# Optimization experiments

Measured on AMD Instinct MI355X. Metric: run time of the kernel, lower is better.

Reference implementation:

```python
import jax, jax.numpy as jnp
import numpy as np
from jax import lax

B, C, H, W = 32, 3, 32, 32
F = 160      # nr_filters
NBLK = 5     # nr_resnet
NMIX = 10    # mixture components
P = 100      # nr_params for 3-channel input


def concat_elu(x):
    return jax.nn.elu(jnp.concatenate([x, -x], axis=1))


def _conv(x, w, b, pad):
    y = lax.conv_general_dilated(x, w, (1, 1), pad, dimension_numbers=('NCHW', 'OIHW', 'NCHW'))
    return y + b[None, :, None, None]


def ds_conv(x, w, b):
    # down-shifted conv: causal in vertical direction
    kh, kw = w.shape[2], w.shape[3]
    return _conv(x, w, b, ((kh - 1, 0), ((kw - 1) // 2, (kw - 1) // 2)))


def dr_conv(x, w, b):
    # down-right-shifted conv: causal in vertical and horizontal direction
    kh, kw = w.shape[2], w.shape[3]
    return _conv(x, w, b, ((kh - 1, 0), (kw - 1, 0)))


def down_shift(x):
    return jnp.pad(x, ((0, 0), (0, 0), (1, 0), (0, 0)))[:, :, :-1, :]


def right_shift(x):
    return jnp.pad(x, ((0, 0), (0, 0), (0, 0), (1, 0)))[:, :, :, :-1]


def nin(x, w, b):
    return jnp.einsum('bchw,oc->bohw', x, w) + b[None, :, None, None]


def gated_resnet(x, a, c1w, c1b, ninw, ninb, c2w, c2b, conv_fn):
    c1 = conv_fn(concat_elu(x), c1w, c1b)
    if a is not None:
        c1 = c1 + nin(concat_elu(a), ninw, ninb)
    c2 = conv_fn(concat_elu(c1), c2w, c2b)  # 2F channels
    g1, g2 = jnp.split(c2, 2, axis=1)
    return x + g1 * jax.nn.sigmoid(g2)


def dmll(x, l):
    # discretized mixture logistic loss; x: [B,C,H,W] in [-1,1], l: [B,P,H,W]
    x = jnp.transpose(x, (0, 2, 3, 1))   # BHWC
    l = jnp.transpose(l, (0, 2, 3, 1))   # BHWP
    logit_probs = l[..., :NMIX]
    rest = l[..., NMIX:].reshape(l.shape[:3] + (C, 3 * NMIX))
    means = rest[..., :NMIX]
    log_scales = jnp.maximum(rest[..., NMIX:2 * NMIX], -7.0)
    coeffs = jnp.tanh(rest[..., 2 * NMIX:])
    xe = x[..., None]                    # BHWC1
    m1 = means[..., 0, :]
    m2 = means[..., 1, :] + coeffs[..., 0, :] * xe[..., 0, :]
    m3 = means[..., 2, :] + coeffs[..., 1, :] * xe[..., 0, :] + coeffs[..., 2, :] * xe[..., 1, :]
    means = jnp.stack([m1, m2, m3], axis=3)  # BHWCM
    centered = xe - means
    inv_stdv = jnp.exp(-log_scales)
    plus_in = inv_stdv * (centered + 1.0 / 255.0)
    min_in = inv_stdv * (centered - 1.0 / 255.0)
    cdf_delta = jax.nn.sigmoid(plus_in) - jax.nn.sigmoid(min_in)
    log_cdf_plus = plus_in - jax.nn.softplus(plus_in)
    log_one_minus_cdf_min = -jax.nn.softplus(min_in)
    mid_in = inv_stdv * centered
    log_pdf_mid = mid_in - log_scales - 2.0 * jax.nn.softplus(mid_in)
    log_probs = jnp.where(xe < -0.999, log_cdf_plus,
                jnp.where(xe > 0.999, log_one_minus_cdf_min,
                jnp.where(cdf_delta > 1e-5, jnp.log(jnp.maximum(cdf_delta, 1e-12)),
                          log_pdf_mid - np.float32(np.log(127.5)))))
    log_probs = log_probs.sum(axis=3) + jax.nn.log_softmax(logit_probs, axis=-1)
    return -jnp.sum(jax.nn.logsumexp(log_probs, axis=-1))


def _forward(samples, w_u_init, b_u_init, w_ul_d, b_ul_d, w_ul_dr, b_ul_dr,
             u_c1_w, u_c1_b, u_c2_w, u_c2_b,
             ul_c1_w, ul_c1_b, ul_nin_w, ul_nin_b, ul_c2_w, ul_c2_b,
             nin_out_w, nin_out_b):
    x = samples * 2.0 - 1.0
    # PixelCNN++ pads a constant ones channel onto the input
    xp = jnp.concatenate([x, jnp.ones_like(x[:, :1])], axis=1)
    u = down_shift(ds_conv(xp, w_u_init, b_u_init))
    ul = down_shift(ds_conv(xp, w_ul_d, b_ul_d)) + right_shift(dr_conv(xp, w_ul_dr, b_ul_dr))
    for i in range(NBLK):
        u = gated_resnet(u, None, u_c1_w[i], u_c1_b[i], None, None, u_c2_w[i], u_c2_b[i], ds_conv)
        ul = gated_resnet(ul, u, ul_c1_w[i], ul_c1_b[i], ul_nin_w[i], ul_nin_b[i], ul_c2_w[i], ul_c2_b[i], dr_conv)
    params = nin(jax.nn.elu(ul), nin_out_w, nin_out_b)  # [B,P,H,W]
    return -dmll(x, params)  # log_prob (scalar, summed over batch/pixels)


def setup_inputs() -> dict:
    key = jax.random.key(0)
    ks = jax.random.split(key, 12)
    s = 0.05
    return {
        'samples': jax.random.uniform(ks[0], (B, C, H, W), jnp.float32),
        'w_u_init': jax.random.normal(ks[1], (F, C + 1, 2, 3), jnp.float32) * s,
        'b_u_init': jnp.zeros((F,), jnp.float32),
        'w_ul_d': jax.random.normal(ks[2], (F, C + 1, 1, 3), jnp.float32) * s,
        'b_ul_d': jnp.zeros((F,), jnp.float32),
        'w_ul_dr': jax.random.normal(ks[3], (F, C + 1, 2, 1), jnp.float32) * s,
        'b_ul_dr': jnp.zeros((F,), jnp.float32),
        'u_c1_w': jax.random.normal(ks[4], (NBLK, F, 2 * F, 2, 3), jnp.float32) * s,
        'u_c1_b': jnp.zeros((NBLK, F), jnp.float32),
        'u_c2_w': jax.random.normal(ks[5], (NBLK, 2 * F, 2 * F, 2, 3), jnp.float32) * s,
        'u_c2_b': jnp.zeros((NBLK, 2 * F), jnp.float32),
        'ul_c1_w': jax.random.normal(ks[6], (NBLK, F, 2 * F, 2, 2), jnp.float32) * s,
        'ul_c1_b': jnp.zeros((NBLK, F), jnp.float32),
        'ul_nin_w': jax.random.normal(ks[7], (NBLK, F, 2 * F), jnp.float32) * s,
        'ul_nin_b': jnp.zeros((NBLK, F), jnp.float32),
        'ul_c2_w': jax.random.normal(ks[8], (NBLK, 2 * F, 2 * F, 2, 2), jnp.float32) * s,
        'ul_c2_b': jnp.zeros((NBLK, 2 * F), jnp.float32),
        'nin_out_w': jax.random.normal(ks[9], (P, F), jnp.float32) * s,
        'nin_out_b': jnp.zeros((P,), jnp.float32),
    }


def reference(samples, w_u_init, b_u_init, w_ul_d, b_ul_d, w_ul_dr, b_ul_dr,
              u_c1_w, u_c1_b, u_c2_w, u_c2_b,
              ul_c1_w, ul_c1_b, ul_nin_w, ul_nin_b, ul_c2_w, ul_c2_b,
              nin_out_w, nin_out_b):
    return _forward(samples, w_u_init, b_u_init, w_ul_d, b_ul_d, w_ul_dr, b_ul_dr,
                    u_c1_w, u_c1_b, u_c2_w, u_c2_b,
                    ul_c1_w, ul_c1_b, ul_nin_w, ul_nin_b, ul_c2_w, ul_c2_b,
                    nin_out_w, nin_out_b)
```

## Files before the change

### kernel.cpp

```cpp
#include <hip/hip_runtime.h>
#include <math.h>

#define BZ 32
#define FCH 160
#define NMIX 10
#define PCH 100

typedef __attribute__((ext_vector_type(8))) short bf16x8;
typedef __attribute__((ext_vector_type(8))) unsigned short u16x8;
typedef __attribute__((ext_vector_type(4))) unsigned short u16x4;
typedef __attribute__((ext_vector_type(4))) float f32x4;

__device__ __forceinline__ unsigned short f2bf(float f) {
    union { float f; unsigned u; } x; x.f = f;
    return (unsigned short)((x.u + 0x7FFFu + ((x.u >> 16) & 1u)) >> 16);
}
__device__ __forceinline__ void elupair(float v, float& e0, float& e1) {
    if (v > 0.f) { e0 = v; e1 = expm1f(-v); }
    else         { e0 = expm1f(v); e1 = -v; }
}
__device__ __forceinline__ int fsw(int p) { return (p + (p >> 2)) & 3; }
__device__ __forceinline__ int swz(int p, int seg) {
    return p * 32 + ((seg ^ fsw(p)) << 3);
}
__device__ __forceinline__ void load_lds16(const unsigned short* g, unsigned short* l) {
    __builtin_amdgcn_global_load_lds(
        (const __attribute__((address_space(1))) unsigned int*)g,
        (__attribute__((address_space(3))) unsigned int*)l, 16, 0, 0);
}

__global__ __launch_bounds__(256) void repack_k(
    const float* __restrict__ w, unsigned short* __restrict__ wb,
    int Cout, int Cin, int NT, int ILV)
{
    __shared__ float ws[1920];
    const int o = blockIdx.x;
    const int nb = blockIdx.y;
    const int CoutPad = gridDim.x;
    const int n = Cin * NT;
    unsigned short* dst = wb + (size_t)(nb * CoutPad + o) * n;
    if (o >= Cout) {
        for (int e = threadIdx.x; e < n; e += 256) dst[e] = 0;
        return;
    }
    const float* src = w + (size_t)(nb * Cout + o) * n;
    for (int e = threadIdx.x; e < n; e += 256) ws[e] = src[e];
    __syncthreads();
    const int half = Cin >> 1;
    for (int e = threadIdx.x; e < n; e += 256) {
        int tap = e / Cin;
        int k = e - tap * Cin;
        int csrc = ILV ? ((k & 1) ? (half + (k >> 1)) : (k >> 1)) : k;
        dst[e] = f2bf(ws[csrc * NT + tap]);
    }
}

__global__ __launch_bounds__(256) void init_both_k(
    const float* __restrict__ smp,
    const float* __restrict__ wu_g, const float* __restrict__ bu_g,
    const float* __restrict__ wd_g, const float* __restrict__ bd_g,
    const float* __restrict__ wr_g, const float* __restrict__ br_g,
    float* __restrict__ u, float* __restrict__ ul,
    unsigned short* __restrict__ ceu, unsigned short* __restrict__ ceul,
    float* __restrict__ zg)
{
    __shared__ float wU[160 * 24];
    __shared__ float wD[160 * 12];
    __shared__ float wR[160 * 8];
    __shared__ float bU[160], bD[160], bR[160];
    __shared__ float X[3][4][34];

    const int tid = threadIdx.x;
    const int i = blockIdx.x;
    const int b = blockIdx.y;

    if (i == 0 && b == 0 && tid < 128) {
        f32x4 z = {0.f, 0.f, 0.f, 0.f};
        ((f32x4*)zg)[tid] = z;
    }

    for (int e = tid; e < 160 * 24; e += 256) wU[e] = wu_g[e];
    for (int e = tid; e < 160 * 12; e += 256) wD[e] = wd_g[e];
    for (int e = tid; e < 160 * 8;  e += 256) wR[e] = wr_g[e];
    if (tid < 160) { bU[tid] = bu_g[tid]; bD[tid] = bd_g[tid]; bR[tid] = br_g[tid]; }
    for (int e = tid; e < 3 * 4 * 34; e += 256) {
        int col = e % 34;
        int c = (e / 34) & 3;
        int rs = e / (34 * 4);
        int r = i - 2 + rs;
        int jj = col - 1;
        float v = 0.f;
        if ((unsigned)r < 32u && (unsigned)jj < 32u)
            v = (c < 3) ? (smp[(((size_t)b * 3 + c) << 10) + (r << 5) + jj] * 2.f - 1.f)
                        : 1.f;
        X[rs][c][col] = v;
    }
    __syncthreads();
    if (tid >= 160) return;
    const int o = tid;

    float wu_r[24], wd_r[12], wr_r[8];
#pragma unroll
    for (int q = 0; q < 24; ++q) wu_r[q] = wU[o * 24 + q];
#pragma unroll
    for (int q = 0; q < 12; ++q) wd_r[q] = wD[o * 12 + q];
#pragma unroll
    for (int q = 0; q < 8; ++q)  wr_r[q] = wR[o * 8 + q];
    const float bu_v = (i > 0) ? bU[o] : 0.f;
    const float bd_v = (i >= 1) ? bD[o] : 0.f;
    const float br_v = bR[o];

    for (int j = 0; j < 32; ++j) {
        float su = 0.f, sd = 0.f, sr = 0.f;
#pragma unroll
        for (int c = 0; c < 4; ++c) {
            float x00 = X[0][c][j], x01 = X[0][c][j + 1], x02 = X[0][c][j + 2];
            float x10 = X[1][c][j], x11 = X[1][c][j + 1], x12 = X[1][c][j + 2];
            float x20 = X[2][c][j];
            su += wu_r[c * 6 + 0] * x00 + wu_r[c * 6 + 1] * x01 + wu_r[c * 6 + 2] * x02
                + wu_r[c * 6 + 3] * x10 + wu_r[c * 6 + 4] * x11 + wu_r[c * 6 + 5] * x12;
            sd += wd_r[c * 3 + 0] * x10 + wd_r[c * 3 + 1] * x11 + wd_r[c * 3 + 2] * x12;
            sr += wr_r[c * 2 + 0] * x10 + wr_r[c * 2 + 1] * x20;
        }
        float uv = (i > 0) ? (su + bu_v) : 0.f;
        float ulv = sd + bd_v + sr + ((j >= 1) ? br_v : 0.f);

        size_t base = (size_t)((b << 10) | (i << 5) | j);
        u[base * 160 + o] = uv;
        ul[base * 160 + o] = ulv;
        float e0, e1;
        elupair(uv, e0, e1);
        unsigned pu = (unsigned)f2bf(e0) | ((unsigned)f2bf(e1) << 16);
        *(unsigned*)(ceu + base * 320 + 2 * o) = pu;
        elupair(ulv, e0, e1);
        unsigned pl = (unsigned)f2bf(e0) | ((unsigned)f2bf(e1) << 16);
        *(unsigned*)(ceul + base * 320 + 2 * o) = pl;
    }
}

template<int KH, int KW, int PT, int PL, bool DUAL, bool GATE, int MBLK>
__global__ __launch_bounds__(256) void conv_mfma_k(
    const unsigned short* __restrict__ cein,
    const unsigned short* __restrict__ wb,
    const unsigned short* __restrict__ cein2,
    const unsigned short* __restrict__ wb2,
    const float* __restrict__ bias, const float* __restrict__ bias2,
    float* __restrict__ resid,
    unsigned short* __restrict__ ceout,
    const unsigned short* __restrict__ zguard)
{
    constexpr int NT = KH * KW;
    constexpr int RW = 8 + KH - 1;
    constexpr int CW = 32 + KW - 1;
    constexpr int MTILES = MBLK / 16;
    constexpr int MSH = (MBLK == 32) ? 5 : 6;
    constexpr int NSA = NT * MBLK / 64;
    constexpr int NSB = (RW * CW * 4 + 255) / 256;

    __shared__ __align__(16) unsigned short bs[NSB * 64 * 32];
    __shared__ __align__(16) unsigned short wsm[NT * MBLK * 32];

    const int tid = threadIdx.x;
    const int wv = tid >> 6;
    const int lane = tid & 63;
    const int l16 = lane & 15;
    const int quad = lane >> 4;

    const int bid = blockIdx.x;
    const int q8 = bid >> 3;
    const int yt = (bid & 7) * 16 + q8 / 5;
    const int m0 = (q8 % 5) * 32;
    const int bimg = yt >> 2;
    const int rowbase = (yt & 3) * 8;

    const int sd = lane & 3;
    const int lr = lane >> 2;

    const unsigned short* srcA[NSA];
#pragma unroll
    for (int it = 0; it < NSA; ++it) {
        int row = it * 64 + wv * 16 + lr;
        int tap = row >> MSH;
        int mm = row & (MBLK - 1);
        int o = GATE ? (mm < 32 ? m0 + mm : 128 + m0 + mm) : (m0 + mm);
        int ss = sd ^ fsw(row);
        srcA[it] = wb + ((size_t)o * NT + tap) * 320 + ss * 8;
    }
    const unsigned short* srcB[NSB];
#pragma unroll
    for (int it = 0; it < NSB; ++it) {
        int p = it * 64 + wv * 16 + lr;
        int r = p / CW;
        int c = p - r * CW;
        int grow = rowbase + r - PT;
        int gcol = c - PL;
        int ss = sd ^ fsw(p);
        bool ok = (p < RW * CW) && ((unsigned)grow < 32u) && ((unsigned)gcol < 32u);
        srcB[it] = ok ? cein + (size_t)(((bimg << 10) | (grow << 5) | gcol)) * 320 + ss * 8
                      : zguard;
    }

    f32x4 acc[MTILES][4];
#pragma unroll
    for (int mt = 0; mt < MTILES; ++mt)
#pragma unroll
        for (int ng = 0; ng < 4; ++ng)
#pragma unroll
            for (int r = 0; r < 4; ++r) acc[mt][ng][r] = 0.f;

    for (int k0 = 0; k0 < 320; k0 += 32) {
        __syncthreads();
#pragma unroll
        for (int it = 0; it < NSB; ++it)
            load_lds16(srcB[it] + k0, &bs[(it * 64 + wv * 16) * 32]);
#pragma unroll
        for (int it = 0; it < NSA; ++it)
            load_lds16(srcA[it] + k0, &wsm[(it * 64 + wv * 16) * 32]);
        __syncthreads();
#pragma unroll
        for (int tap = 0; tap < NT; ++tap) {
            const int kh = tap / KW, kw = tap % KW;
            bf16x8 af[MTILES];
#pragma unroll
            for (int mt = 0; mt < MTILES; ++mt)
                af[mt] = *(const bf16x8*)&wsm[swz(tap * MBLK + mt * 16 + l16, quad)];
#pragma unroll
            for (int ng = 0; ng < 4; ++ng) {
                int rl = 2 * wv + (ng >> 1) + kh;
                int cc = (ng & 1) * 16 + l16 + kw;
                bf16x8 bfr = *(const bf16x8*)&bs[swz(rl * CW + cc, quad)];
#pragma unroll
                for (int mt = 0; mt < MTILES; ++mt)
                    acc[mt][ng] = __builtin_amdgcn_mfma_f32_16x16x32_bf16(af[mt], bfr, acc[mt][ng], 0, 0, 0);
            }
        }
    }

    if (DUAL) {
        const unsigned short* srcB2[4];
#pragma unroll
        for (int it = 0; it < 4; ++it) {
            int p2 = it * 64 + wv * 16 + lr;
            int r = p2 >> 5, c = p2 & 31;
            int ss = sd ^ fsw(p2);
            srcB2[it] = cein2 + (size_t)(((bimg << 10) | ((rowbase + r) << 5) | c)) * 320 + ss * 8;
        }
        int row2 = wv * 16 + lr;
        int mm2 = row2 & 31;
        const unsigned short* srcA2 =
            wb2 + (size_t)(m0 + mm2) * 320 + (sd ^ fsw(row2)) * 8;

        for (int k0 = 0; k0 < 320; k0 += 32) {
            __syncthreads();
#pragma unroll
            for (int it = 0; it < 4; ++it)
                load_lds16(srcB2[it] + k0, &bs[(it * 64 + wv * 16) * 32]);
            if (wv < 2)
                load_lds16(srcA2 + k0, &wsm[(wv * 16) * 32]);
            __syncthreads();
            bf16x8 af[MTILES];
#pragma unroll
            for (int mt = 0; mt < MTILES; ++mt)
                af[mt] = *(const bf16x8*)&wsm[swz(mt * 16 + l16, quad)];
#pragma unroll
            for (int ng = 0; ng < 4; ++ng) {
                int rl = 2 * wv + (ng >> 1);
                int cc = (ng & 1) * 16 + l16;
                bf16x8 bfr = *(const bf16x8*)&bs[swz(rl * 32 + cc, quad)];
#pragma unroll
                for (int mt = 0; mt < MTILES; ++mt)
                    acc[mt][ng] = __builtin_amdgcn_mfma_f32_16x16x32_bf16(af[mt], bfr, acc[mt][ng], 0, 0, 0);
            }
        }
    }

    constexpr int MOUT = GATE ? MTILES / 2 : MTILES;
#pragma unroll
    for (int mt = 0; mt < MOUT; ++mt) {
        int ob = m0 + mt * 16 + quad * 4;
        f32x4 bv = *(const f32x4*)(bias + ob);
        f32x4 bv2;
        if (DUAL) bv2 = *(const f32x4*)(bias2 + ob);
        f32x4 bg;
        if (GATE) bg = *(const f32x4*)(bias + ob + 160);
#pragma unroll
        for (int ng = 0; ng < 4; ++ng) {
            int i = rowbase + 2 * wv + (ng >> 1);
            int j = (ng & 1) * 16 + l16;
            size_t pb = (size_t)((bimg << 10) | (i << 5) | j);
            if (!GATE) {
                u16x8 st;
#pragma unroll
                for (int r = 0; r < 4; ++r) {
                    float v = acc[mt][ng][r] + bv[r] + (DUAL ? bv2[r] : 0.f);
                    float e0, e1; elupair(v, e0, e1);
                    st[2 * r] = f2bf(e0); st[2 * r + 1] = f2bf(e1);
                }
                *(u16x8*)(ceout + pb * 320 + 2 * ob) = st;
            } else {
                f32x4 rv = *(const f32x4*)(resid + pb * 160 + ob);
                u16x8 st;
#pragma unroll
                for (int r = 0; r < 4; ++r) {
                    float g1 = acc[mt][ng][r] + bv[r];
                    float g2 = acc[mt + MTILES / 2][ng][r] + bg[r];
                    float v = rv[r] + g1 / (1.f + expf(-g2));
                    rv[r] = v;
                    float e0, e1; elupair(v, e0, e1);
                    st[2 * r] = f2bf(e0); st[2 * r + 1] = f2bf(e1);
                }
                *(f32x4*)(resid + pb * 160 + ob) = rv;
                *(u16x8*)(ceout + pb * 320 + 2 * ob) = st;
            }
        }
    }
}

__global__ __launch_bounds__(256) void ninout_k(
    const float* __restrict__ ul, const unsigned short* __restrict__ wbn,
    const float* __restrict__ bias, float* __restrict__ params)
{
    constexpr int KCP = 40;
    __shared__ __align__(16) unsigned short bs[256 * KCP];
    __shared__ __align__(16) unsigned short wsm[32 * KCP];

    const int tid = threadIdx.x;
    const int wv = tid >> 6;
    const int lane = tid & 63;
    const int l16 = lane & 15;
    const int quad = lane >> 4;
    const int m0 = blockIdx.x * 32;
    const int bimg = blockIdx.y >> 2;
    const int rowbase = (blockIdx.y & 3) * 8;

    f32x4 acc[2][4];
#pragma unroll
    for (int mt = 0; mt < 2; ++mt)
#pragma unroll
        for (int ng = 0; ng < 4; ++ng)
#pragma unroll
            for (int r = 0; r < 4; ++r) acc[mt][ng][r] = 0.f;

    for (int k0 = 0; k0 < 160; k0 += 32) {
        __syncthreads();
        for (int e = tid; e < 256 * 8; e += 256) {
            int s = e & 7;
            int p = e >> 3;
            int pix = ((rowbase + (p >> 5)) << 5) | (p & 31);
            f32x4 xv = *(const f32x4*)(ul + (size_t)(((bimg << 10) | pix)) * 160 + k0 + s * 4);
            u16x4 st;
#pragma unroll
            for (int t = 0; t < 4; ++t) {
                float v = xv[t];
                st[t] = f2bf(v > 0.f ? v : expm1f(v));
            }
            *(u16x4*)(bs + p * KCP + s * 4) = st;
        }
        for (int e = tid; e < 32 * 4; e += 256) {
            int seg = e & 3;
            int mm = e >> 2;
            bf16x8 v = *(const bf16x8*)(wbn + (size_t)(m0 + mm) * 160 + k0 + seg * 8);
            *(bf16x8*)(wsm + mm * KCP + seg * 8) = v;
        }
        __syncthreads();
        bf16x8 af[2];
#pragma unroll
        for (int mt = 0; mt < 2; ++mt)
            af[mt] = *(const bf16x8*)&wsm[(mt * 16 + l16) * KCP + quad * 8];
#pragma unroll
        for (int ng = 0; ng < 4; ++ng) {
            int rl = 2 * wv + (ng >> 1);
            int cc = (ng & 1) * 16 + l16;
            bf16x8 bfr = *(const bf16x8*)&bs[(rl * 32 + cc) * KCP + quad * 8];
#pragma unroll
            for (int mt = 0; mt < 2; ++mt)
                acc[mt][ng] = __builtin_amdgcn_mfma_f32_16x16x32_bf16(af[mt], bfr, acc[mt][ng], 0, 0, 0);
        }
    }
#pragma unroll
    for (int mt = 0; mt < 2; ++mt)
#pragma unroll
        for (int ng = 0; ng < 4; ++ng) {
            int i = rowbase + 2 * wv + (ng >> 1);
            int j = (ng & 1) * 16 + l16;
            int pix = (i << 5) + j;
#pragma unroll
            for (int r = 0; r < 4; ++r) {
                int o = m0 + mt * 16 + quad * 4 + r;
                if (o < PCH)
                    params[(((size_t)bimg * PCH + o) << 10) + pix] = acc[mt][ng][r] + bias[o];
            }
        }
}

__device__ __forceinline__ float softplus_f(float v) {
    return fmaxf(v, 0.f) + log1pf(expf(-fabsf(v)));
}
__device__ __forceinline__ float sigmoid_f(float v) { return 1.f / (1.f + expf(-v)); }
__device__ __forceinline__ float lpterm(float x, float m, float ls) {
    float inv = expf(-ls);
    float cen = x - m;
    float plus = inv * (cen + 0.00392156862745098f);
    float minv = inv * (cen - 0.00392156862745098f);
    float cdf_delta = sigmoid_f(plus) - sigmoid_f(minv);
    float log_cdf_plus = plus - softplus_f(plus);
    float log_om = -softplus_f(minv);
    float mid = inv * cen;
    float log_pdf_mid = mid - ls - 2.f * softplus_f(mid);
    float inner = (cdf_delta > 1e-5f) ? logf(fmaxf(cdf_delta, 1e-12f))
                                      : (log_pdf_mid - 4.848116389675623f);
    return (x < -0.999f) ? log_cdf_plus : ((x > 0.999f) ? log_om : inner);
}

__global__ __launch_bounds__(256) void dmll_k(
    const float* __restrict__ smp, const float* __restrict__ params,
    float* __restrict__ partials)
{
    const int tid = threadIdx.x;
    const int n = tid & 15;
    const int ploc = tid >> 4;
    const int pix_g = blockIdx.x * 16 + ploc;
    const int b = pix_g >> 10;
    const int ij = pix_g & 1023;
    const float* P = params + ((size_t)b * PCH << 10) + ij;

    float x0 = smp[(((size_t)b * 3 + 0) << 10) + ij] * 2.f - 1.f;
    float x1 = smp[(((size_t)b * 3 + 1) << 10) + ij] * 2.f - 1.f;
    float x2 = smp[(((size_t)b * 3 + 2) << 10) + ij] * 2.f - 1.f;

    float logit = -1e30f;
    if (n < NMIX) logit = P[(size_t)n << 10];
    float mx = logit;
#pragma unroll
    for (int m = 1; m < 16; m <<= 1) mx = fmaxf(mx, __shfl_xor(mx, m, 16));
    float ex = (n < NMIX) ? expf(logit - mx) : 0.f;
    float se = ex;
#pragma unroll
    for (int m = 1; m < 16; m <<= 1) se += __shfl_xor(se, m, 16);
    float lse_logit = mx + logf(se);

    float lp = -1e30f;
    if (n < NMIX) {
        float mean0 = P[(size_t)(10 + n) << 10];
        float mean1 = P[(size_t)(40 + n) << 10];
        float mean2 = P[(size_t)(70 + n) << 10];
        float ls0 = fmaxf(P[(size_t)(20 + n) << 10], -7.f);
        float ls1 = fmaxf(P[(size_t)(50 + n) << 10], -7.f);
        float ls2 = fmaxf(P[(size_t)(80 + n) << 10], -7.f);
        float c0 = tanhf(P[(size_t)(30 + n) << 10]);
        float c1 = tanhf(P[(size_t)(60 + n) << 10]);
        float c2 = tanhf(P[(size_t)(90 + n) << 10]);
        float m0 = mean0;
        float m1 = mean1 + c0 * x0;
        float m2 = mean2 + c1 * x0 + c2 * x1;
        float s3 = lpterm(x0, m0, ls0) + lpterm(x1, m1, ls1) + lpterm(x2, m2, ls2);
        lp = s3 + logit - lse_logit;
    }
    float mx2 = lp;
#pragma unroll
    for (int m = 1; m < 16; m <<= 1) mx2 = fmaxf(mx2, __shfl_xor(mx2, m, 16));
    float e2 = (n < NMIX) ? expf(lp - mx2) : 0.f;
    float se2 = e2;
#pragma unroll
    for (int m = 1; m < 16; m <<= 1) se2 += __shfl_xor(se2, m, 16);
    float v = (n == 0) ? (mx2 + logf(se2)) : 0.f;

#pragma unroll
    for (int off = 32; off > 0; off >>= 1) v += __shfl_down(v, off);
    __shared__ float red[4];
    if ((tid & 63) == 0) red[tid >> 6] = v;
    __syncthreads();
    if (tid == 0) partials[blockIdx.x] = red[0] + red[1] + red[2] + red[3];
}

__global__ __launch_bounds__(256) void dmll_final_k(
    const float* __restrict__ partials, float* __restrict__ out)
{
    float v = 0.f;
    for (int k = threadIdx.x; k < 2048; k += 256) v += partials[k];
#pragma unroll
    for (int off = 32; off > 0; off >>= 1) v += __shfl_down(v, off);
    __shared__ float red[4];
    if ((threadIdx.x & 63) == 0) red[threadIdx.x >> 6] = v;
    __syncthreads();
    if (threadIdx.x == 0) out[0] = red[0] + red[1] + red[2] + red[3];
}

extern "C" void kernel_launch(void* const* d_in, const int* in_sizes, int n_in,
                              void* d_out, int out_size, void* d_ws, size_t ws_size,
                              hipStream_t stream)
{
    const float* samples   = (const float*)d_in[0];
    const float* w_u_init  = (const float*)d_in[1];
    const float* b_u_init  = (const float*)d_in[2];
    const float* w_ul_d    = (const float*)d_in[3];
    const float* b_ul_d    = (const float*)d_in[4];
    const float* w_ul_dr   = (const float*)d_in[5];
    const float* b_ul_dr   = (const float*)d_in[6];
    const float* u_c1_w    = (const float*)d_in[7];
    const float* u_c1_b    = (const float*)d_in[8];
    const float* u_c2_w    = (const float*)d_in[9];
    const float* u_c2_b    = (const float*)d_in[10];
    const float* ul_c1_w   = (const float*)d_in[11];
    const float* ul_c1_b   = (const float*)d_in[12];
    const float* ul_nin_w  = (const float*)d_in[13];
    const float* ul_nin_b  = (const float*)d_in[14];
    const float* ul_c2_w   = (const float*)d_in[15];
    const float* ul_c2_b   = (const float*)d_in[16];
    const float* nin_out_w = (const float*)d_in[17];
    const float* nin_out_b = (const float*)d_in[18];
    float* out = (float*)d_out;

    const size_t NU = (size_t)BZ * FCH * 1024;
    float* u  = (float*)d_ws;
    float* ul = u + NU;
    unsigned short* CEu  = (unsigned short*)(ul + NU);
    unsigned short* CEc1 = CEu + 2 * NU;
    unsigned short* CEul = CEc1 + 2 * NU;
    unsigned short* WBu1  = CEul + 2 * NU;
    unsigned short* WBu2  = WBu1 + (size_t)5 * 160 * 6 * 320;
    unsigned short* WBul1 = WBu2 + (size_t)5 * 320 * 6 * 320;
    unsigned short* WBnin = WBul1 + (size_t)5 * 160 * 4 * 320;
    unsigned short* WBul2 = WBnin + (size_t)5 * 160 * 1 * 320;
    unsigned short* WBnout = WBul2 + (size_t)5 * 320 * 4 * 320;
    float* partials = (float*)(WBnout + (size_t)128 * 160);
    float* zguard = partials + 2048;
    float* params = (float*)CEc1;

    dim3 blk(256);

    repack_k<<<dim3(160, 5), blk, 0, stream>>>(u_c1_w,    WBu1,  160, 320, 6, 1);
    repack_k<<<dim3(320, 5), blk, 0, stream>>>(u_c2_w,    WBu2,  320, 320, 6, 1);
    repack_k<<<dim3(160, 5), blk, 0, stream>>>(ul_c1_w,   WBul1, 160, 320, 4, 1);
    repack_k<<<dim3(160, 5), blk, 0, stream>>>(ul_nin_w,  WBnin, 160, 320, 1, 1);
    repack_k<<<dim3(320, 5), blk, 0, stream>>>(ul_c2_w,   WBul2, 320, 320, 4, 1);
    repack_k<<<dim3(128, 1), blk, 0, stream>>>(nin_out_w, WBnout, 100, 160, 1, 0);

    init_both_k<<<dim3(32, 32), blk, 0, stream>>>(
        samples, w_u_init, b_u_init, w_ul_d, b_ul_d, w_ul_dr, b_ul_dr,
        u, ul, CEu, CEul, zguard);

    const unsigned short* zg = (const unsigned short*)zguard;
    for (int t = 0; t < 5; ++t) {
        conv_mfma_k<2, 3, 1, 1, false, false, 32><<<640, blk, 0, stream>>>(
            CEu, WBu1 + (size_t)t * 160 * 6 * 320, nullptr, nullptr,
            u_c1_b + t * 160, nullptr, nullptr, CEc1, zg);
        conv_mfma_k<2, 3, 1, 1, false, true, 64><<<640, blk, 0, stream>>>(
            CEc1, WBu2 + (size_t)t * 320 * 6 * 320, nullptr, nullptr,
            u_c2_b + t * 320, nullptr, u, CEu, zg);
        conv_mfma_k<2, 2, 1, 1, true, false, 32><<<640, blk, 0, stream>>>(
            CEul, WBul1 + (size_t)t * 160 * 4 * 320, CEu, WBnin + (size_t)t * 160 * 320,
            ul_c1_b + t * 160, ul_nin_b + t * 160, nullptr, CEc1, zg);
        conv_mfma_k<2, 2, 1, 1, false, true, 64><<<640, blk, 0, stream>>>(
            CEc1, WBul2 + (size_t)t * 320 * 4 * 320, nullptr, nullptr,
            ul_c2_b + t * 320, nullptr, ul, CEul, zg);
    }

    ninout_k<<<dim3(4, 128), blk, 0, stream>>>(ul, WBnout, nin_out_b, params);
    dmll_k<<<2048, blk, 0, stream>>>(samples, params, partials);
    dmll_final_k<<<1, 256, 0, stream>>>(partials, out);
}
```

Baseline: 1.114 ms.

## Skew u and ul resnet streams to co-launch their conv stages

The up stream (u) is run one block ahead of the up-left stream (ul). Each pair of independent convolutions, ul block t and u block t+1, now runs in one kernel launch of 1280 workgroups that branches on block index. The conv body becomes a device function using dynamic shared memory. Separate c1 scratch buffers are added for each stream. This cuts the number of conv launches and doubles the grid per launch, to reduce launch gaps and partial-wave tails, at the cost of extra workspace and mixed-shape workgroups in one grid.

```diff
diff --git a/kernel.cpp b/kernel.cpp
--- a/kernel.cpp
+++ b/kernel.cpp
@@ -139,7 +139,8 @@
 }
 
 template<int KH, int KW, int PT, int PL, bool DUAL, bool GATE, int MBLK>
-__global__ __launch_bounds__(256) void conv_mfma_k(
+__device__ __forceinline__ void conv_body(
+    int bid, unsigned short* smem,
     const unsigned short* __restrict__ cein,
     const unsigned short* __restrict__ wb,
     const unsigned short* __restrict__ cein2,
@@ -156,9 +157,10 @@
     constexpr int MSH = (MBLK == 32) ? 5 : 6;
     constexpr int NSA = NT * MBLK / 64;
     constexpr int NSB = (RW * CW * 4 + 255) / 256;
-
-    __shared__ __align__(16) unsigned short bs[NSB * 64 * 32];
-    __shared__ __align__(16) unsigned short wsm[NT * MBLK * 32];
+    constexpr int BSZ = NSB * 64 * 32;
+
+    unsigned short* bs = smem;
+    unsigned short* wsm = smem + BSZ;
 
     const int tid = threadIdx.x;
     const int wv = tid >> 6;
@@ -166,7 +168,6 @@
     const int l16 = lane & 15;
     const int quad = lane >> 4;
 
-    const int bid = blockIdx.x;
     const int q8 = bid >> 3;
     const int yt = (bid & 7) * 16 + q8 / 5;
     const int m0 = (q8 % 5) * 32;
@@ -314,6 +315,55 @@
             }
         }
     }
+}
+
+template<int KH, int KW, int PT, int PL, bool DUAL, bool GATE, int MBLK>
+__global__ __launch_bounds__(256) void conv_single_k(
+    const unsigned short* __restrict__ cein, const unsigned short* __restrict__ wb,
+    const unsigned short* __restrict__ cein2, const unsigned short* __restrict__ wb2,
+    const float* __restrict__ bias, const float* __restrict__ bias2,
+    float* __restrict__ resid, unsigned short* __restrict__ ceout,
+    const unsigned short* __restrict__ zguard)
+{
+    extern __shared__ __align__(16) unsigned short dsm[];
+    conv_body<KH, KW, PT, PL, DUAL, GATE, MBLK>(
+        blockIdx.x, dsm, cein, wb, cein2, wb2, bias, bias2, resid, ceout, zguard);
+}
+
+__global__ __launch_bounds__(256) void conv_fused_c1_k(
+    const unsigned short* __restrict__ ceul, const unsigned short* __restrict__ wul1,
+    const unsigned short* __restrict__ ceu_nin, const unsigned short* __restrict__ wnin,
+    const float* __restrict__ bul1, const float* __restrict__ bnin,
+    unsigned short* __restrict__ cec1ul,
+    const unsigned short* __restrict__ ceu, const unsigned short* __restrict__ wu1,
+    const float* __restrict__ bu1, unsigned short* __restrict__ cec1u,
+    const unsigned short* __restrict__ zguard)
+{
+    extern __shared__ __align__(16) unsigned short dsm[];
+    if (blockIdx.x < 640)
+        conv_body<2, 2, 1, 1, true, false, 32>(
+            blockIdx.x, dsm, ceul, wul1, ceu_nin, wnin, bul1, bnin, nullptr, cec1ul, zguard);
+    else
+        conv_body<2, 3, 1, 1, false, false, 32>(
+            blockIdx.x - 640, dsm, ceu, wu1, nullptr, nullptr, bu1, nullptr, nullptr, cec1u, zguard);
+}
+
+__global__ __launch_bounds__(256) void conv_fused_c2_k(
+    const unsigned short* __restrict__ cec1ul, const unsigned short* __restrict__ wul2,
+    const float* __restrict__ bul2, float* __restrict__ ul_r,
+    unsigned short* __restrict__ ceul,
+    const unsigned short* __restrict__ cec1u, const unsigned short* __restrict__ wu2,
+    const float* __restrict__ bu2, float* __restrict__ u_r,
+    unsigned short* __restrict__ ceu,
+    const unsigned short* __restrict__ zguard)
+{
+    extern __shared__ __align__(16) unsigned short dsm[];
+    if (blockIdx.x < 640)
+        conv_body<2, 2, 1, 1, false, true, 64>(
+            blockIdx.x, dsm, cec1ul, wul2, nullptr, nullptr, bul2, nullptr, ul_r, ceul, zguard);
+    else
+        conv_body<2, 3, 1, 1, false, true, 64>(
+            blockIdx.x - 640, dsm, cec1u, wu2, nullptr, nullptr, bu2, nullptr, u_r, ceu, zguard);
 }
 
 __global__ __launch_bounds__(256) void ninout_k(
@@ -514,9 +564,10 @@
     const size_t NU = (size_t)BZ * FCH * 1024;
     float* u  = (float*)d_ws;
     float* ul = u + NU;
-    unsigned short* CEu  = (unsigned short*)(ul + NU);
-    unsigned short* CEc1 = CEu + 2 * NU;
-    unsigned short* CEul = CEc1 + 2 * NU;
+    unsigned short* CEu    = (unsigned short*)(ul + NU);
+    unsigned short* CEc1u  = CEu + 2 * NU;
+    unsigned short* CEc1ul = CEc1u + 2 * NU;
+    unsigned short* CEul   = CEc1ul + 2 * NU;
     unsigned short* WBu1  = CEul + 2 * NU;
     unsigned short* WBu2  = WBu1 + (size_t)5 * 160 * 6 * 320;
     unsigned short* WBul1 = WBu2 + (size_t)5 * 320 * 6 * 320;
@@ -525,9 +576,16 @@
     unsigned short* WBnout = WBul2 + (size_t)5 * 320 * 4 * 320;
     float* partials = (float*)(WBnout + (size_t)128 * 160);
     float* zguard = partials + 2048;
-    float* params = (float*)CEc1;
+    float* params = (float*)CEc1u;
 
     dim3 blk(256);
+
+    const int SH_UC1  = (5 * 64 * 32 + 6 * 32 * 32) * 2;
+    const int SH_UC2  = (5 * 64 * 32 + 6 * 64 * 32) * 2;
+    const int SH_ULC1 = (5 * 64 * 32 + 4 * 32 * 32) * 2;
+    const int SH_ULC2 = (5 * 64 * 32 + 4 * 64 * 32) * 2;
+    const int SH_F1 = SH_UC1;
+    const int SH_F2 = SH_UC2;
 
     repack_k<<<dim3(160, 5), blk, 0, stream>>>(u_c1_w,    WBu1,  160, 320, 6, 1);
     repack_k<<<dim3(320, 5), blk, 0, stream>>>(u_c2_w,    WBu2,  320, 320, 6, 1);
@@ -541,20 +599,32 @@
         u, ul, CEu, CEul, zguard);
 
     const unsigned short* zg = (const unsigned short*)zguard;
-    for (int t = 0; t < 5; ++t) {
-        conv_mfma_k<2, 3, 1, 1, false, false, 32><<<640, blk, 0, stream>>>(
-            CEu, WBu1 + (size_t)t * 160 * 6 * 320, nullptr, nullptr,
-            u_c1_b + t * 160, nullptr, nullptr, CEc1, zg);
-        conv_mfma_k<2, 3, 1, 1, false, true, 64><<<640, blk, 0, stream>>>(
-            CEc1, WBu2 + (size_t)t * 320 * 6 * 320, nullptr, nullptr,
-            u_c2_b + t * 320, nullptr, u, CEu, zg);
-        conv_mfma_k<2, 2, 1, 1, true, false, 32><<<640, blk, 0, stream>>>(
-            CEul, WBul1 + (size_t)t * 160 * 4 * 320, CEu, WBnin + (size_t)t * 160 * 320,
-            ul_c1_b + t * 160, ul_nin_b + t * 160, nullptr, CEc1, zg);
-        conv_mfma_k<2, 2, 1, 1, false, true, 64><<<640, blk, 0, stream>>>(
-            CEc1, WBul2 + (size_t)t * 320 * 4 * 320, nullptr, nullptr,
-            ul_c2_b + t * 320, nullptr, ul, CEul, zg);
-    }
+
+    conv_single_k<2, 3, 1, 1, false, false, 32><<<640, blk, SH_UC1, stream>>>(
+        CEu, WBu1, nullptr, nullptr, u_c1_b, nullptr, nullptr, CEc1u, zg);
+    conv_single_k<2, 3, 1, 1, false, true, 64><<<640, blk, SH_UC2, stream>>>(
+        CEc1u, WBu2, nullptr, nullptr, u_c2_b, nullptr, u, CEu, zg);
+
+    for (int t = 0; t < 4; ++t) {
+        conv_fused_c1_k<<<1280, blk, SH_F1, stream>>>(
+            CEul, WBul1 + (size_t)t * 160 * 4 * 320,
+            CEu, WBnin + (size_t)t * 160 * 320,
+            ul_c1_b + t * 160, ul_nin_b + t * 160, CEc1ul,
+            CEu, WBu1 + (size_t)(t + 1) * 160 * 6 * 320,
+            u_c1_b + (t + 1) * 160, CEc1u, zg);
+        conv_fused_c2_k<<<1280, blk, SH_F2, stream>>>(
+            CEc1ul, WBul2 + (size_t)t * 320 * 4 * 320,
+            ul_c2_b + t * 320, ul, CEul,
+            CEc1u, WBu2 + (size_t)(t + 1) * 320 * 6 * 320,
+            u_c2_b + (t + 1) * 320, u, CEu, zg);
+    }
+
+    conv_single_k<2, 2, 1, 1, true, false, 32><<<640, blk, SH_ULC1, stream>>>(
+        CEul, WBul1 + (size_t)4 * 160 * 4 * 320, CEu, WBnin + (size_t)4 * 160 * 320,
+        ul_c1_b + 4 * 160, ul_nin_b + 4 * 160, nullptr, CEc1ul, zg);
+    conv_single_k<2, 2, 1, 1, false, true, 64><<<640, blk, SH_ULC2, stream>>>(
+        CEc1ul, WBul2 + (size_t)4 * 320 * 4 * 320, nullptr, nullptr,
+        ul_c2_b + 4 * 320, nullptr, ul, CEul, zg);
 
     ninout_k<<<dim3(4, 128), blk, 0, stream>>>(ul, WBnout, nin_out_b, params);
     dmll_k<<<2048, blk, 0, stream>>>(samples, params, partials);
```

Measured after the change: 987.2 us, median of 3. 11.4% less time.
